# Performance work log

Hardware: AMD Instinct MI355X
Metric: run time of the kernel (lower is better)

## Reference

```python
import jax, jax.numpy as jnp
import numpy as np

N_NODES = 50000
N_EDGES = 800000
D_IN, D_HID, D_OUT = 96, 96, 48


def _gcn_conv(x, src, dst, W, b, num_nodes):
    """PyG GCNConv: h = x @ W; out[dst] += norm * h[src]; out += b.
    Symmetric normalization deg^{-1/2}[src] * deg^{-1/2}[dst], self-loops included
    (src/dst already contain self-loops)."""
    h = x @ W  # [N, d_out]
    deg = jax.ops.segment_sum(jnp.ones_like(dst, dtype=h.dtype), dst,
                              num_segments=num_nodes)  # in-degree incl. self-loop
    dinv = jnp.where(deg > 0, jax.lax.rsqrt(deg), 0.0)
    norm = dinv[src] * dinv[dst]  # [E+N]
    msgs = h[src] * norm[:, None]  # gather + scale (the memory-bound part)
    out = jax.ops.segment_sum(msgs, dst, num_segments=num_nodes)  # scatter-add
    return out + b


def setup_inputs() -> dict:
    key = jax.random.key(0)
    k1, k2, k3, k4 = jax.random.split(key, 4)
    x = jax.random.normal(k1, (N_NODES, D_IN), dtype=jnp.float32)
    edge_index = jax.random.randint(k2, (2, N_EDGES), 0, N_NODES, dtype=jnp.int64)
    # Glorot-ish init for weights, zero bias (matches GCNConv defaults)
    W1 = jax.random.normal(k3, (D_IN, D_HID), dtype=jnp.float32) / np.sqrt(D_IN)
    b1 = jnp.zeros((D_HID,), dtype=jnp.float32)
    W2 = jax.random.normal(k4, (D_HID, D_OUT), dtype=jnp.float32) / np.sqrt(D_HID)
    b2 = jnp.zeros((D_OUT,), dtype=jnp.float32)
    return {"x": x, "edge_index": edge_index, "W1": W1, "b1": b1, "W2": W2, "b2": b2}


def reference(x, edge_index, W1, b1, W2, b2):
    num_nodes = x.shape[0]
    loops = jnp.arange(num_nodes, dtype=edge_index.dtype)
    src = jnp.concatenate([edge_index[0], loops])  # add self-loops
    dst = jnp.concatenate([edge_index[1], loops])
    h = _gcn_conv(x, src, dst, W1, b1, num_nodes)
    h = jax.nn.relu(h)
    # dropout p=0.5 is identity in eval mode (self.training=False)
    out = _gcn_conv(h, src, dst, W2, b2, num_nodes)
    return out
```

## Files before the change

kernel.cpp:

```cpp
#include <hip/hip_runtime.h>
#include <hip/hip_bf16.h>


constexpr int NN = 50000;
constexpr int NE = 800000;
constexpr int DI = 96;
constexpr int DH = 96;
constexpr int DO = 48;

constexpr int BK_SHIFT = 6;
constexpr int NBK      = (NN + 63) >> 6;
constexpr int BK_CAP   = 2048;

constexpr int NCHUNK = 128;
constexpr int CH     = (NE + NCHUNK - 1) / NCHUNK;

typedef unsigned short ushort8 __attribute__((ext_vector_type(8)));

__device__ __forceinline__ float bf2f(unsigned short u) {
    return __uint_as_float(((unsigned int)u) << 16);
}


__global__ __launch_bounds__(256) void k_hist(const int* __restrict__ dst,
                                              int* __restrict__ C, int e) {
    __shared__ int hist[NBK];
    for (int i = threadIdx.x; i < NBK; i += 256) hist[i] = 0;
    __syncthreads();
    const int blk = blockIdx.x;
    const int beg = blk * CH, end = min(beg + CH, e);
    for (int i = beg + threadIdx.x; i < end; i += 256)
        atomicAdd(&hist[dst[i] >> BK_SHIFT], 1);
    __syncthreads();
    for (int b = threadIdx.x; b < NBK; b += 256)
        C[b * NCHUNK + blk] = hist[b];
}

__global__ __launch_bounds__(256) void k_rowscan(int* __restrict__ C,
                                                 int* __restrict__ totals) {
    const int w    = threadIdx.x >> 6;
    const int lane = threadIdx.x & 63;
    const int r    = blockIdx.x * 4 + w;
    if (r >= NBK) return;
    int* row = C + r * NCHUNK;
    const int v0 = row[lane];
    const int v1 = row[64 + lane];
    int s0 = v0, s1 = v1;
#pragma unroll
    for (int off = 1; off < 64; off <<= 1) {
        int y0 = __shfl_up(s0, off);
        int y1 = __shfl_up(s1, off);
        if (lane >= off) { s0 += y0; s1 += y1; }
    }
    s1 += __shfl(s0, 63);
    row[lane]      = s0 - v0;
    row[64 + lane] = s1 - v1;
    if (lane == 63) totals[r] = s1;
}

__global__ __launch_bounds__(1024) void k_scan_base(const int* __restrict__ totals,
                                                    int* __restrict__ bk_ptr,
                                                    int* __restrict__ row_ptr) {
    __shared__ int sh[1024];
    const int t = threadIdx.x;
    const int v = (t < NBK) ? totals[t] : 0;
    sh[t] = v;
    __syncthreads();
#pragma unroll
    for (int off = 1; off < 1024; off <<= 1) {
        int x = sh[t];
        int a = (t >= off) ? sh[t - off] : 0;
        __syncthreads();
        sh[t] = x + a;
        __syncthreads();
    }
    if (t < NBK) bk_ptr[t] = sh[t] - v;
    if (t == 0) { bk_ptr[NBK] = NE; row_ptr[NN] = NE; }
}

__global__ __launch_bounds__(256) void k_scatter(const int* __restrict__ src,
                                                 const int* __restrict__ dst,
                                                 const int* __restrict__ C,
                                                 const int* __restrict__ bk_ptr,
                                                 unsigned* __restrict__ ebuf, int e) {
    __shared__ int cur[NBK];
    const int blk = blockIdx.x;
    for (int b = threadIdx.x; b < NBK; b += 256)
        cur[b] = bk_ptr[b] + C[b * NCHUNK + blk];
    __syncthreads();
    const int beg = blk * CH, end = min(beg + CH, e);
    for (int i = beg + threadIdx.x; i < end; i += 256) {
        int d = dst[i];
        int b = d >> BK_SHIFT;
        int pos = atomicAdd(&cur[b], 1);
        ebuf[pos] = ((unsigned)(d & 63) << 16) | (unsigned)src[i];
    }
}

__global__ __launch_bounds__(256) void k_bsort(const unsigned* __restrict__ ebuf,
                                               const int* __restrict__ bk_ptr,
                                               int* __restrict__ row_ptr,
                                               float* __restrict__ dinv,
                                               int* __restrict__ src_sorted, int n) {
    __shared__ unsigned eL[BK_CAP];
    __shared__ int outL[BK_CAP];
    __shared__ int curL[64];
    __shared__ int baseL[64];

    const int b   = blockIdx.x;
    const int beg = bk_ptr[b];
    const int m   = bk_ptr[b + 1] - beg;
    const int t   = threadIdx.x;

    if (t < 64) curL[t] = 0;
    __syncthreads();

    for (int i = t; i < m; i += 256) {
        unsigned v = ebuf[beg + i];
        eL[i] = v;
        atomicAdd(&curL[v >> 16], 1);
    }
    __syncthreads();

    if (t < 64) {
        int c = curL[t];
        int x = c;
#pragma unroll
        for (int off = 1; off < 64; off <<= 1) {
            int y = __shfl_up(x, off);
            if (t >= off) x += y;
        }
        int excl = x - c;
        baseL[t] = excl;
        int d0 = (b << BK_SHIFT) + t;
        if (d0 < n) {
            row_ptr[d0] = beg + excl;
            dinv[d0]    = rsqrtf((float)(c + 1));
        }
    }
    __syncthreads();
    if (t < 64) curL[t] = baseL[t];
    __syncthreads();

    for (int i = t; i < m; i += 256) {
        unsigned v = eL[i];
        int p = atomicAdd(&curL[v >> 16], 1);
        outL[p] = (int)(v & 0xFFFFu);
    }
    __syncthreads();
    for (int i = t; i < m; i += 256) src_sorted[beg + i] = outL[i];
}


template<int DOUT>
__global__ __launch_bounds__(256) void k_gemm(const float* __restrict__ X,
                                              const float* __restrict__ W,
                                              const float* __restrict__ dinv,
                                              __hip_bfloat16* __restrict__ H, int n) {
    constexpr int ROWS = 32;
    constexpr int CPT  = DOUT / 16;
    constexpr int RPT  = 2;

    __shared__ float ws[DI * DOUT];
    __shared__ float xs[ROWS][DI];

    const int tid  = threadIdx.x;
    const int row0 = blockIdx.x * ROWS;

    for (int i = tid; i < DI * DOUT; i += 256) ws[i] = W[i];

    {
        const float4* Xv  = reinterpret_cast<const float4*>(X + (size_t)row0 * DI);
        float4*       xsv = reinterpret_cast<float4*>(&xs[0][0]);
        const int nv   = ROWS * DI / 4;
        const int maxv = ((n - row0) * DI) / 4;
        for (int i = tid; i < nv; i += 256) {
            float4 v = (i < maxv) ? Xv[i] : float4{0.f, 0.f, 0.f, 0.f};
            xsv[i] = v;
        }
    }
    __syncthreads();

    const int cg = tid & 15;
    const int rg = tid >> 4;

    float acc[RPT][CPT];
#pragma unroll
    for (int i = 0; i < RPT; ++i)
#pragma unroll
        for (int j = 0; j < CPT; ++j) acc[i][j] = 0.f;

    for (int k = 0; k < DI; ++k) {
        float xv[RPT];
#pragma unroll
        for (int i = 0; i < RPT; ++i) xv[i] = xs[rg * RPT + i][k];
#pragma unroll
        for (int j = 0; j < CPT; ++j) {
            float wv = ws[k * DOUT + cg * CPT + j];
#pragma unroll
            for (int i = 0; i < RPT; ++i) acc[i][j] += xv[i] * wv;
        }
    }

#pragma unroll
    for (int i = 0; i < RPT; ++i) {
        int row = row0 + rg * RPT + i;
        if (row < n) {
            float dv = dinv[row];
#pragma unroll
            for (int j = 0; j < CPT; ++j)
                H[(size_t)row * DOUT + cg * CPT + j] = __float2bfloat16(acc[i][j] * dv);
        }
    }
}


template<int D, bool RELU>
__global__ __launch_bounds__(256) void k_agg_csr(const unsigned short* __restrict__ h,
                                                 const float* __restrict__ dinv,
                                                 const int* __restrict__ row_ptr,
                                                 const int* __restrict__ src_sorted,
                                                 const float* __restrict__ bias,
                                                 float* __restrict__ out, int n) {
    constexpr int G = D / 8;
    int t = blockIdx.x * blockDim.x + threadIdx.x;
    if (t >= n * G) return;
    const int node = t / G;
    const int g    = t % G;

    const ushort8* h8 = reinterpret_cast<const ushort8*>(h);

    float accA[8], accB[8];
    {
        ushort8 hv = h8[(size_t)node * G + g];
#pragma unroll
        for (int j = 0; j < 8; ++j) { accA[j] = bf2f(hv[j]); accB[j] = 0.f; }
    }

    const int beg = row_ptr[node];
    const int end = row_ptr[node + 1];
    int k = beg;
    for (; k + 4 <= end; k += 4) {
        int s0 = src_sorted[k + 0];
        int s1 = src_sorted[k + 1];
        int s2 = src_sorted[k + 2];
        int s3 = src_sorted[k + 3];
        ushort8 v0 = h8[(size_t)s0 * G + g];
        ushort8 v1 = h8[(size_t)s1 * G + g];
        ushort8 v2 = h8[(size_t)s2 * G + g];
        ushort8 v3 = h8[(size_t)s3 * G + g];
#pragma unroll
        for (int j = 0; j < 8; ++j) {
            accA[j] += bf2f(v0[j]) + bf2f(v1[j]);
            accB[j] += bf2f(v2[j]) + bf2f(v3[j]);
        }
    }
    for (; k < end; ++k) {
        int s = src_sorted[k];
        ushort8 v = h8[(size_t)s * G + g];
#pragma unroll
        for (int j = 0; j < 8; ++j) accA[j] += bf2f(v[j]);
    }

    const float di = dinv[node];
    const float4* b4 = reinterpret_cast<const float4*>(bias);
    float4 b0 = b4[g * 2], b1 = b4[g * 2 + 1];
    float r[8];
#pragma unroll
    for (int j = 0; j < 8; ++j) r[j] = di * (accA[j] + accB[j]);
    r[0] += b0.x; r[1] += b0.y; r[2] += b0.z; r[3] += b0.w;
    r[4] += b1.x; r[5] += b1.y; r[6] += b1.z; r[7] += b1.w;
    if (RELU) {
#pragma unroll
        for (int j = 0; j < 8; ++j) r[j] = fmaxf(r[j], 0.f);
    }
    float4* o4 = reinterpret_cast<float4*>(out + (size_t)node * D + g * 8);
    o4[0] = float4{r[0], r[1], r[2], r[3]};
    o4[1] = float4{r[4], r[5], r[6], r[7]};
}


extern "C" void kernel_launch(void* const* d_in, const int* in_sizes, int n_in,
                              void* d_out, int out_size, void* d_ws, size_t ws_size,
                              hipStream_t stream) {
    const float* x   = (const float*)d_in[0];
    const int*   ei  = (const int*)d_in[1];
    const float* W1  = (const float*)d_in[2];
    const float* b1  = (const float*)d_in[3];
    const float* W2  = (const float*)d_in[4];
    const float* b2  = (const float*)d_in[5];
    float*       out = (float*)d_out;

    const int* srcv = ei;
    const int* dstv = ei + NE;

    char* p = (char*)d_ws;
    float*          dinv  = (float*)p;          p += (size_t)NN * 4;
    float*          a1    = (float*)p;          p += (size_t)NN * DH * 4;
    __hip_bfloat16* h1    = (__hip_bfloat16*)p; p += (size_t)NN * DH * 2;
    int*      row_ptr     = (int*)p;            p += (size_t)(NN + 1) * 4;
    int*      src_sorted  = (int*)p;            p += (size_t)NE * 4;
    unsigned* ebuf        = (unsigned*)p;       p += (size_t)NE * 4;
    int*      Cm          = (int*)p;            p += (size_t)NBK * NCHUNK * 4;
    int*      totals      = (int*)p;            p += (size_t)NBK * 4;
    int*      bk_ptr      = (int*)p;            p += (size_t)(NBK + 1) * 4;

    const int B = 256;

    k_hist<<<NCHUNK, B, 0, stream>>>(dstv, Cm, NE);
    k_rowscan<<<(NBK + 3) / 4, B, 0, stream>>>(Cm, totals);
    k_scan_base<<<1, 1024, 0, stream>>>(totals, bk_ptr, row_ptr);
    k_scatter<<<NCHUNK, B, 0, stream>>>(srcv, dstv, Cm, bk_ptr, ebuf, NE);
    k_bsort<<<NBK, B, 0, stream>>>(ebuf, bk_ptr, row_ptr, dinv, src_sorted, NN);

    k_gemm<DH><<<(NN + 31) / 32, B, 0, stream>>>(x, W1, dinv, h1, NN);
    {
        int total = NN * (DH / 8);
        k_agg_csr<DH, true><<<(total + B - 1) / B, B, 0, stream>>>(
            (const unsigned short*)h1, dinv, row_ptr, src_sorted, b1, a1, NN);
    }

    __hip_bfloat16* h2 = h1;
    k_gemm<DO><<<(NN + 31) / 32, B, 0, stream>>>(a1, W2, dinv, h2, NN);
    {
        int total = NN * (DO / 8);
        k_agg_csr<DO, false><<<(total + B - 1) / B, B, 0, stream>>>(
            (const unsigned short*)h2, dinv, row_ptr, src_sorted, b2, out, NN);
    }
}
```

Baseline: 129.9 us.

## Store hidden activations in bf16, fold base scan into scatter, vectorize index loads

The layer-1 aggregation output is now written as bf16 and read as bf16 by the second GEMM, which halves that intermediate's traffic. The separate single-block bucket-offset scan kernel is removed: each scatter block recomputes the prefix over bucket totals in shared memory, and block 0 writes bk_ptr. The aggregation loop aligns to 4 edges and loads source indices as int4. The bf16 hidden state adds rounding error, and every scatter block now repeats the same scan.

```diff
diff --git a/kernel.cpp b/kernel.cpp
--- a/kernel.cpp
+++ b/kernel.cpp
@@ -20,6 +20,10 @@
 __device__ __forceinline__ float bf2f(unsigned short u) {
     return __uint_as_float(((unsigned int)u) << 16);
 }
+__device__ __forceinline__ unsigned short f2bf(float f) {
+    __hip_bfloat16 b = __float2bfloat16(f);
+    return *reinterpret_cast<unsigned short*>(&b);
+}
 
 
 __global__ __launch_bounds__(256) void k_hist(const int* __restrict__ dst,
@@ -37,7 +41,9 @@
 }
 
 __global__ __launch_bounds__(256) void k_rowscan(int* __restrict__ C,
-                                                 int* __restrict__ totals) {
+                                                 int* __restrict__ totals,
+                                                 int* __restrict__ row_ptr) {
+    if (blockIdx.x == 0 && threadIdx.x == 0) row_ptr[NN] = NE;
     const int w    = threadIdx.x >> 6;
     const int lane = threadIdx.x & 63;
     const int r    = blockIdx.x * 4 + w;
@@ -58,38 +64,53 @@
     if (lane == 63) totals[r] = s1;
 }
 
-__global__ __launch_bounds__(1024) void k_scan_base(const int* __restrict__ totals,
-                                                    int* __restrict__ bk_ptr,
-                                                    int* __restrict__ row_ptr) {
-    __shared__ int sh[1024];
-    const int t = threadIdx.x;
-    const int v = (t < NBK) ? totals[t] : 0;
-    sh[t] = v;
-    __syncthreads();
-#pragma unroll
-    for (int off = 1; off < 1024; off <<= 1) {
-        int x = sh[t];
-        int a = (t >= off) ? sh[t - off] : 0;
-        __syncthreads();
-        sh[t] = x + a;
-        __syncthreads();
-    }
-    if (t < NBK) bk_ptr[t] = sh[t] - v;
-    if (t == 0) { bk_ptr[NBK] = NE; row_ptr[NN] = NE; }
-}
-
 __global__ __launch_bounds__(256) void k_scatter(const int* __restrict__ src,
                                                  const int* __restrict__ dst,
                                                  const int* __restrict__ C,
-                                                 const int* __restrict__ bk_ptr,
+                                                 const int* __restrict__ totals,
+                                                 int* __restrict__ bk_ptr,
                                                  unsigned* __restrict__ ebuf, int e) {
+    __shared__ int bkL[NBK + 1];
+    __shared__ int part[256];
     __shared__ int cur[NBK];
+    const int t = threadIdx.x;
+
+    int v[4];
+    int s = 0;
+    const int base = t * 4;
+#pragma unroll
+    for (int i = 0; i < 4; ++i) {
+        int idx = base + i;
+        v[i] = (idx < NBK) ? totals[idx] : 0;
+        s += v[i];
+    }
+    part[t] = s;
+    __syncthreads();
+#pragma unroll
+    for (int off = 1; off < 256; off <<= 1) {
+        int x = part[t];
+        int a = (t >= off) ? part[t - off] : 0;
+        __syncthreads();
+        part[t] = x + a;
+        __syncthreads();
+    }
+    int run = part[t] - s;
+#pragma unroll
+    for (int i = 0; i < 4; ++i) {
+        int idx = base + i;
+        if (idx <= NBK) bkL[idx] = run;
+        run += v[i];
+    }
+    __syncthreads();
+
     const int blk = blockIdx.x;
-    for (int b = threadIdx.x; b < NBK; b += 256)
-        cur[b] = bk_ptr[b] + C[b * NCHUNK + blk];
-    __syncthreads();
+    for (int b = t; b < NBK; b += 256) cur[b] = bkL[b] + C[b * NCHUNK + blk];
+    if (blk == 0)
+        for (int i = t; i <= NBK; i += 256) bk_ptr[i] = bkL[i];
+    __syncthreads();
+
     const int beg = blk * CH, end = min(beg + CH, e);
-    for (int i = beg + threadIdx.x; i < end; i += 256) {
+    for (int i = beg + t; i < end; i += 256) {
         int d = dst[i];
         int b = d >> BK_SHIFT;
         int pos = atomicAdd(&cur[b], 1);
@@ -152,32 +173,41 @@
 }
 
 
-template<int DOUT>
-__global__ __launch_bounds__(256) void k_gemm(const float* __restrict__ X,
+template<int DOUT, bool XBF16>
+__global__ __launch_bounds__(256) void k_gemm(const void* __restrict__ Xin,
                                               const float* __restrict__ W,
                                               const float* __restrict__ dinv,
-                                              __hip_bfloat16* __restrict__ H, int n) {
+                                              unsigned short* __restrict__ H, int n) {
     constexpr int ROWS = 32;
     constexpr int CPT  = DOUT / 16;
     constexpr int RPT  = 2;
 
     __shared__ float ws[DI * DOUT];
-    __shared__ float xs[ROWS][DI];
+    __shared__ unsigned char xraw[ROWS * DI * (XBF16 ? 2 : 4)];
+    float*          xsf = reinterpret_cast<float*>(xraw);
+    unsigned short* xsu = reinterpret_cast<unsigned short*>(xraw);
 
     const int tid  = threadIdx.x;
     const int row0 = blockIdx.x * ROWS;
 
     for (int i = tid; i < DI * DOUT; i += 256) ws[i] = W[i];
 
-    {
-        const float4* Xv  = reinterpret_cast<const float4*>(X + (size_t)row0 * DI);
-        float4*       xsv = reinterpret_cast<float4*>(&xs[0][0]);
+    if (XBF16) {
+        const ushort8* Xv = reinterpret_cast<const ushort8*>(
+            (const unsigned short*)Xin + (size_t)row0 * DI);
+        ushort8* xv = reinterpret_cast<ushort8*>(xsu);
+        const int nv   = ROWS * DI / 8;
+        const int maxv = ((n - row0) * DI) / 8;
+        for (int i = tid; i < nv; i += 256)
+            xv[i] = (i < maxv) ? Xv[i] : (ushort8)(0);
+    } else {
+        const float4* Xv = reinterpret_cast<const float4*>(
+            (const float*)Xin + (size_t)row0 * DI);
+        float4* xv = reinterpret_cast<float4*>(xsf);
         const int nv   = ROWS * DI / 4;
         const int maxv = ((n - row0) * DI) / 4;
-        for (int i = tid; i < nv; i += 256) {
-            float4 v = (i < maxv) ? Xv[i] : float4{0.f, 0.f, 0.f, 0.f};
-            xsv[i] = v;
-        }
+        for (int i = tid; i < nv; i += 256)
+            xv[i] = (i < maxv) ? Xv[i] : float4{0.f, 0.f, 0.f, 0.f};
     }
     __syncthreads();
 
@@ -193,7 +223,10 @@
     for (int k = 0; k < DI; ++k) {
         float xv[RPT];
 #pragma unroll
-        for (int i = 0; i < RPT; ++i) xv[i] = xs[rg * RPT + i][k];
+        for (int i = 0; i < RPT; ++i) {
+            int r = rg * RPT + i;
+            xv[i] = XBF16 ? bf2f(xsu[r * DI + k]) : xsf[r * DI + k];
+        }
 #pragma unroll
         for (int j = 0; j < CPT; ++j) {
             float wv = ws[k * DOUT + cg * CPT + j];
@@ -209,19 +242,19 @@
             float dv = dinv[row];
 #pragma unroll
             for (int j = 0; j < CPT; ++j)
-                H[(size_t)row * DOUT + cg * CPT + j] = __float2bfloat16(acc[i][j] * dv);
-        }
-    }
-}
-
-
-template<int D, bool RELU>
+                H[(size_t)row * DOUT + cg * CPT + j] = f2bf(acc[i][j] * dv);
+        }
+    }
+}
+
+
+template<int D, bool RELU, bool OUTBF16>
 __global__ __launch_bounds__(256) void k_agg_csr(const unsigned short* __restrict__ h,
                                                  const float* __restrict__ dinv,
                                                  const int* __restrict__ row_ptr,
                                                  const int* __restrict__ src_sorted,
                                                  const float* __restrict__ bias,
-                                                 float* __restrict__ out, int n) {
+                                                 void* __restrict__ outp, int n) {
     constexpr int G = D / 8;
     int t = blockIdx.x * blockDim.x + threadIdx.x;
     if (t >= n * G) return;
@@ -240,15 +273,20 @@
     const int beg = row_ptr[node];
     const int end = row_ptr[node + 1];
     int k = beg;
+    int kA = min((beg + 3) & ~3, end);
+    for (; k < kA; ++k) {
+        int s = src_sorted[k];
+        ushort8 vv = h8[(size_t)s * G + g];
+#pragma unroll
+        for (int j = 0; j < 8; ++j) accA[j] += bf2f(vv[j]);
+    }
+    const int4* sv = reinterpret_cast<const int4*>(src_sorted + k);
     for (; k + 4 <= end; k += 4) {
-        int s0 = src_sorted[k + 0];
-        int s1 = src_sorted[k + 1];
-        int s2 = src_sorted[k + 2];
-        int s3 = src_sorted[k + 3];
-        ushort8 v0 = h8[(size_t)s0 * G + g];
-        ushort8 v1 = h8[(size_t)s1 * G + g];
-        ushort8 v2 = h8[(size_t)s2 * G + g];
-        ushort8 v3 = h8[(size_t)s3 * G + g];
+        int4 s4 = *sv++;
+        ushort8 v0 = h8[(size_t)s4.x * G + g];
+        ushort8 v1 = h8[(size_t)s4.y * G + g];
+        ushort8 v2 = h8[(size_t)s4.z * G + g];
+        ushort8 v3 = h8[(size_t)s4.w * G + g];
 #pragma unroll
         for (int j = 0; j < 8; ++j) {
             accA[j] += bf2f(v0[j]) + bf2f(v1[j]);
@@ -257,9 +295,9 @@
     }
     for (; k < end; ++k) {
         int s = src_sorted[k];
-        ushort8 v = h8[(size_t)s * G + g];
-#pragma unroll
-        for (int j = 0; j < 8; ++j) accA[j] += bf2f(v[j]);
+        ushort8 vv = h8[(size_t)s * G + g];
+#pragma unroll
+        for (int j = 0; j < 8; ++j) accA[j] += bf2f(vv[j]);
     }
 
     const float di = dinv[node];
@@ -274,9 +312,16 @@
 #pragma unroll
         for (int j = 0; j < 8; ++j) r[j] = fmaxf(r[j], 0.f);
     }
-    float4* o4 = reinterpret_cast<float4*>(out + (size_t)node * D + g * 8);
-    o4[0] = float4{r[0], r[1], r[2], r[3]};
-    o4[1] = float4{r[4], r[5], r[6], r[7]};
+    if (OUTBF16) {
+        ushort8 o;
+#pragma unroll
+        for (int j = 0; j < 8; ++j) o[j] = f2bf(r[j]);
+        reinterpret_cast<ushort8*>((unsigned short*)outp)[(size_t)node * G + g] = o;
+    } else {
+        float4* o4 = reinterpret_cast<float4*>((float*)outp + (size_t)node * D + g * 8);
+        o4[0] = float4{r[0], r[1], r[2], r[3]};
+        o4[1] = float4{r[4], r[5], r[6], r[7]};
+    }
 }
 
 
@@ -295,36 +340,35 @@
     const int* dstv = ei + NE;
 
     char* p = (char*)d_ws;
-    float*          dinv  = (float*)p;          p += (size_t)NN * 4;
-    float*          a1    = (float*)p;          p += (size_t)NN * DH * 4;
-    __hip_bfloat16* h1    = (__hip_bfloat16*)p; p += (size_t)NN * DH * 2;
-    int*      row_ptr     = (int*)p;            p += (size_t)(NN + 1) * 4;
-    int*      src_sorted  = (int*)p;            p += (size_t)NE * 4;
-    unsigned* ebuf        = (unsigned*)p;       p += (size_t)NE * 4;
-    int*      Cm          = (int*)p;            p += (size_t)NBK * NCHUNK * 4;
-    int*      totals      = (int*)p;            p += (size_t)NBK * 4;
-    int*      bk_ptr      = (int*)p;            p += (size_t)(NBK + 1) * 4;
+    float*          dinv  = (float*)p;           p += (size_t)NN * 4;
+    unsigned short* a1    = (unsigned short*)p;  p += (size_t)NN * DH * 2;
+    unsigned short* h1    = (unsigned short*)p;  p += (size_t)NN * DH * 2;
+    int*      row_ptr     = (int*)p;             p += (size_t)(NN + 16) * 4;
+    int*      src_sorted  = (int*)p;             p += (size_t)NE * 4;
+    unsigned* ebuf        = (unsigned*)p;        p += (size_t)NE * 4;
+    int*      Cm          = (int*)p;             p += (size_t)NBK * NCHUNK * 4;
+    int*      totals      = (int*)p;             p += (size_t)NBK * 4;
+    int*      bk_ptr      = (int*)p;             p += (size_t)(NBK + 1) * 4;
 
     const int B = 256;
 
     k_hist<<<NCHUNK, B, 0, stream>>>(dstv, Cm, NE);
-    k_rowscan<<<(NBK + 3) / 4, B, 0, stream>>>(Cm, totals);
-    k_scan_base<<<1, 1024, 0, stream>>>(totals, bk_ptr, row_ptr);
-    k_scatter<<<NCHUNK, B, 0, stream>>>(srcv, dstv, Cm, bk_ptr, ebuf, NE);
+    k_rowscan<<<(NBK + 3) / 4, B, 0, stream>>>(Cm, totals, row_ptr);
+    k_scatter<<<NCHUNK, B, 0, stream>>>(srcv, dstv, Cm, totals, bk_ptr, ebuf, NE);
     k_bsort<<<NBK, B, 0, stream>>>(ebuf, bk_ptr, row_ptr, dinv, src_sorted, NN);
 
-    k_gemm<DH><<<(NN + 31) / 32, B, 0, stream>>>(x, W1, dinv, h1, NN);
+    k_gemm<DH, false><<<(NN + 31) / 32, B, 0, stream>>>(x, W1, dinv, h1, NN);
     {
         int total = NN * (DH / 8);
-        k_agg_csr<DH, true><<<(total + B - 1) / B, B, 0, stream>>>(
-            (const unsigned short*)h1, dinv, row_ptr, src_sorted, b1, a1, NN);
-    }
-
-    __hip_bfloat16* h2 = h1;
-    k_gemm<DO><<<(NN + 31) / 32, B, 0, stream>>>(a1, W2, dinv, h2, NN);
+        k_agg_csr<DH, true, true><<<(total + B - 1) / B, B, 0, stream>>>(
+            h1, dinv, row_ptr, src_sorted, b1, a1, NN);
+    }
+
+    unsigned short* h2 = h1;
+    k_gemm<DO, true><<<(NN + 31) / 32, B, 0, stream>>>(a1, W2, dinv, h2, NN);
     {
         int total = NN * (DO / 8);
-        k_agg_csr<DO, false><<<(total + B - 1) / B, B, 0, stream>>>(
-            (const unsigned short*)h2, dinv, row_ptr, src_sorted, b2, out, NN);
-    }
-}
+        k_agg_csr<DO, false, false><<<(total + B - 1) / B, B, 0, stream>>>(
+            h2, dinv, row_ptr, src_sorted, b2, out, NN);
+    }
+}
```

New measurement: 127.3 us. Within noise of the previous version (-2.0%).
